# Kernel optimization log

Hardware: AMD Instinct MI355X
Metric: run time of the kernel (lower is better)

The kernel has to match this reference:

```python
import jax, jax.numpy as jnp
import numpy as np

B, S, D_IN, D_OUT, H = 2, 2048, 1024, 1024, 16
DK = D_OUT // H


def setup_inputs() -> dict:
    key = jax.random.key(0)
    ks = jax.random.split(key, 6)
    s_in = 1.0 / np.sqrt(D_IN)
    s_out = 1.0 / np.sqrt(D_OUT)
    return {
        "x": jax.random.normal(ks[0], (B, S, D_IN), dtype=jnp.float32),
        "Wq": jax.random.uniform(ks[1], (D_OUT, D_IN), jnp.float32, -s_in, s_in),
        "Wk": jax.random.uniform(ks[2], (D_OUT, D_IN), jnp.float32, -s_in, s_in),
        "Wv": jax.random.uniform(ks[3], (D_OUT, D_IN), jnp.float32, -s_in, s_in),
        "Wo": jax.random.uniform(ks[4], (D_OUT, D_OUT), jnp.float32, -s_out, s_out),
        "bo": jax.random.uniform(ks[5], (D_OUT,), jnp.float32, -s_out, s_out),
    }


def reference(x, Wq, Wk, Wv, Wo, bo):
    b, s, _ = x.shape
    # torch Linear: y = x @ W.T
    q = (x @ Wq.T).reshape(b, s, H, DK).transpose(0, 2, 1, 3)  # [b,h,s,dk]
    k = (x @ Wk.T).reshape(b, s, H, DK).transpose(0, 2, 1, 3)
    v = (x @ Wv.T).reshape(b, s, H, DK).transpose(0, 2, 1, 3)
    scores = jnp.einsum("bhqd,bhkd->bhqk", q, k)
    causal = jnp.tril(jnp.ones((s, s), dtype=bool))  # True = keep
    scores = jnp.where(causal, scores, -jnp.inf)
    attn = jax.nn.softmax(scores / np.sqrt(DK), axis=-1)
    # dropout p=0.0 (eval) -> identity
    ctx = jnp.einsum("bhqk,bhkd->bhqd", attn, v)
    ctx = ctx.transpose(0, 2, 1, 3).reshape(b, s, D_OUT)
    return ctx @ Wo.T + bo
```

## Files before the change

kernel.cpp:

```cpp
#include <hip/hip_runtime.h>
#include <stdint.h>

#define B_   2
#define S_   2048
#define DIN  1024
#define DOUT 1024
#define H_   16
#define DK_  64
#define MSZ  (B_ * S_)

typedef __bf16 bf16v8 __attribute__((ext_vector_type(8)));
typedef float  f32x4  __attribute__((ext_vector_type(4)));

__device__ __forceinline__ ushort f2b(float f) {
  union { float f; uint32_t u; } a; a.f = f;
  uint32_t u = a.u;
  u += 0x7FFFu + ((u >> 16) & 1u);
  return (ushort)(u >> 16);
}

__device__ __forceinline__ uint32_t pk2(float lo, float hi) {
  union { __bf16 h; ushort u; } a, b;
  a.h = (__bf16)lo; b.h = (__bf16)hi;
  return (uint32_t)a.u | ((uint32_t)b.u << 16);
}

#define GLDS(gp, lp) __builtin_amdgcn_global_load_lds(                         \
    (const __attribute__((address_space(1))) void*)(gp),                       \
    (__attribute__((address_space(3))) void*)(lp), 16, 0, 0)

__global__ void cvt_all(const float* __restrict__ x,  const float* __restrict__ wq,
                        const float* __restrict__ wk, const float* __restrict__ wv,
                        const float* __restrict__ wo,
                        ushort* __restrict__ xb,  ushort* __restrict__ wqb,
                        ushort* __restrict__ wkb, ushort* __restrict__ wvb,
                        ushort* __restrict__ wob) {
  int i = blockIdx.x * blockDim.x + threadIdx.x;
  const int NX = 1 << 20, NW = 1 << 18;
  const float* src; ushort* dst; int off;
  if (i < NX)               { src = x;  dst = xb;  off = i; }
  else if (i < NX + NW)     { src = wq; dst = wqb; off = i - NX; }
  else if (i < NX + 2 * NW) { src = wk; dst = wkb; off = i - NX - NW; }
  else if (i < NX + 3 * NW) { src = wv; dst = wvb; off = i - NX - 2 * NW; }
  else                      { src = wo; dst = wob; off = i - NX - 3 * NW; }
  float4 v = reinterpret_cast<const float4*>(src)[off];
  ushort4 o;
  o.x = f2b(v.x); o.y = f2b(v.y); o.z = f2b(v.z); o.w = f2b(v.w);
  reinterpret_cast<ushort4*>(dst)[off] = o;
}

__global__ __launch_bounds__(256)
void gemm_qkv(const ushort* __restrict__ A,
              const ushort* __restrict__ Bq, const ushort* __restrict__ Bk,
              const ushort* __restrict__ Bv,
              ushort* __restrict__ Oq, ushort* __restrict__ Ok,
              ushort* __restrict__ Vt, int M, int K) {
  __shared__ ushort sA[128 * 64];
  __shared__ ushort sB[128 * 64];

  const int tid  = threadIdx.x;
  const int lane = tid & 63, wid = tid >> 6;
  const int wr = wid >> 1, wc = wid & 1;
  const int g = lane >> 4, c = lane & 15;
  const int m0 = blockIdx.x * 128;

  const int wsel = blockIdx.y >> 3;
  const int n0w  = (blockIdx.y & 7) * 128;
  const ushort* Bm = (wsel == 0) ? Bq : (wsel == 1) ? Bk : Bv;

  const int msk = (c & 7) << 4;

  f32x4 acc[4][4] = {};

  for (int k0 = 0; k0 < K; k0 += 64) {
    __syncthreads();
#pragma unroll
    for (int i = 0; i < 4; ++i) {
      int idx = i * 256 + tid;
      int row = idx >> 3;
      int scol = (((idx & 7) ^ (row & 7)) << 3);
      GLDS(A  + (size_t)(m0 + row) * K + k0 + scol, (char*)sA + idx * 16);
      GLDS(Bm + (size_t)(n0w + row) * K + k0 + scol, (char*)sB + idx * 16);
    }
    __syncthreads();

    bf16v8 aF[4][2], bF[4][2];
#pragma unroll
    for (int m = 0; m < 4; ++m) {
      const char* rp = (const char*)sA + (wr * 64 + m * 16 + c) * 128;
#pragma unroll
      for (int ks = 0; ks < 2; ++ks)
        aF[m][ks] = *reinterpret_cast<const bf16v8*>(rp + ((ks * 64 + g * 16) ^ msk));
    }
#pragma unroll
    for (int n = 0; n < 4; ++n) {
      const char* rp = (const char*)sB + (wc * 64 + n * 16 + c) * 128;
#pragma unroll
      for (int ks = 0; ks < 2; ++ks)
        bF[n][ks] = *reinterpret_cast<const bf16v8*>(rp + ((ks * 64 + g * 16) ^ msk));
    }
#pragma unroll
    for (int m = 0; m < 4; ++m)
#pragma unroll
      for (int n = 0; n < 4; ++n) {
        acc[m][n] = __builtin_amdgcn_mfma_f32_16x16x32_bf16(aF[m][0], bF[n][0], acc[m][n], 0, 0, 0);
        acc[m][n] = __builtin_amdgcn_mfma_f32_16x16x32_bf16(aF[m][1], bF[n][1], acc[m][n], 0, 0, 0);
      }
  }

  __syncthreads();

  if (wsel == 2) {
#pragma unroll
    for (int m = 0; m < 4; ++m)
#pragma unroll
      for (int n = 0; n < 4; ++n) {
        int row0 = m0 + wr * 64 + g * 4 + m * 16;
        int col  = n0w + wc * 64 + c + n * 16;
        int bb = row0 >> 11, ss = row0 & 2047;
        int hh = col >> 6, dd = col & 63;
        ushort4 o4;
        o4.x = f2b(acc[m][n][0]); o4.y = f2b(acc[m][n][1]);
        o4.z = f2b(acc[m][n][2]); o4.w = f2b(acc[m][n][3]);
        *reinterpret_cast<ushort4*>(
            &Vt[((size_t)(bb * 16 + hh) * 64 + dd) * 2048 + ss]) = o4;
      }
  } else {
    const float oscale = (wsel == 0) ? 0.125f * 1.4426950408889634f : 1.0f;
    ushort* Ob = (wsel == 0) ? Oq : Ok;
    char* eb = (char*)sA + wid * 2048;
#pragma unroll
    for (int m = 0; m < 4; ++m) {
#pragma unroll
      for (int n = 0; n < 4; ++n)
#pragma unroll
        for (int i = 0; i < 4; ++i) {
          int prow = g * 4 + i;
          *(ushort*)(eb + prow * 128 + ((n * 32 + c * 2) ^ ((prow & 7) << 4))) =
              f2b(acc[m][n][i] * oscale);
        }
      const int r = lane >> 2, cq = lane & 3;
      const int m2 = (r & 7) << 4;
      bf16v8 t0 = *reinterpret_cast<const bf16v8*>(eb + r * 128 + ((cq * 32) ^ m2));
      bf16v8 t1 = *reinterpret_cast<const bf16v8*>(eb + r * 128 + ((cq * 32 + 16) ^ m2));
      ushort* Gb = Ob + (size_t)(m0 + wr * 64 + m * 16 + r) * DOUT +
                   n0w + wc * 64 + cq * 16;
      *reinterpret_cast<bf16v8*>(Gb) = t0;
      *reinterpret_cast<bf16v8*>(Gb + 8) = t1;
    }
  }
}

__global__ __launch_bounds__(256)
void gemm_proj(const ushort* __restrict__ A, const ushort* __restrict__ Bw,
               float* __restrict__ Cf, const float* __restrict__ bias,
               int M, int K) {
  __shared__ ushort sAB[2][64 * 64];

  const int tid  = threadIdx.x;
  const int lane = tid & 63, wid = tid >> 6;
  const int wr = wid >> 1, wc = wid & 1;
  const int g = lane >> 4, c = lane & 15;
  const int m0 = blockIdx.x * 64, n0 = blockIdx.y * 64;

  const int msk = (c & 7) << 4;

  f32x4 acc[2][2] = {};

  for (int k0 = 0; k0 < K; k0 += 64) {
    __syncthreads();
#pragma unroll
    for (int i = 0; i < 2; ++i) {
      int idx = i * 256 + tid;
      int row = idx >> 3;
      int scol = (((idx & 7) ^ (row & 7)) << 3);
      GLDS(A  + (size_t)(m0 + row) * K + k0 + scol, (char*)&sAB[0][0] + idx * 16);
      GLDS(Bw + (size_t)(n0 + row) * K + k0 + scol, (char*)&sAB[1][0] + idx * 16);
    }
    __syncthreads();

    bf16v8 aF[2][2], bF[2][2];
#pragma unroll
    for (int m = 0; m < 2; ++m) {
      const char* rp = (const char*)&sAB[0][0] + (wr * 32 + m * 16 + c) * 128;
#pragma unroll
      for (int ks = 0; ks < 2; ++ks)
        aF[m][ks] = *reinterpret_cast<const bf16v8*>(rp + ((ks * 64 + g * 16) ^ msk));
    }
#pragma unroll
    for (int n = 0; n < 2; ++n) {
      const char* rp = (const char*)&sAB[1][0] + (wc * 32 + n * 16 + c) * 128;
#pragma unroll
      for (int ks = 0; ks < 2; ++ks)
        bF[n][ks] = *reinterpret_cast<const bf16v8*>(rp + ((ks * 64 + g * 16) ^ msk));
    }
#pragma unroll
    for (int m = 0; m < 2; ++m)
#pragma unroll
      for (int n = 0; n < 2; ++n) {
        acc[m][n] = __builtin_amdgcn_mfma_f32_16x16x32_bf16(aF[m][0], bF[n][0], acc[m][n], 0, 0, 0);
        acc[m][n] = __builtin_amdgcn_mfma_f32_16x16x32_bf16(aF[m][1], bF[n][1], acc[m][n], 0, 0, 0);
      }
  }

  __syncthreads();

  float bv[2];
#pragma unroll
  for (int n = 0; n < 2; ++n) bv[n] = bias[n0 + wc * 32 + n * 16 + c];

  float* ef = (float*)((char*)&sAB[0][0] + wid * 4096);
#pragma unroll
  for (int m = 0; m < 2; ++m)
#pragma unroll
    for (int n = 0; n < 2; ++n)
#pragma unroll
      for (int i = 0; i < 4; ++i) {
        int row = m * 16 + g * 4 + i;
        ef[row * 32 + ((n * 16 + c) ^ ((row & 7) << 2))] = acc[m][n][i] + bv[n];
      }
#pragma unroll
  for (int pass = 0; pass < 4; ++pass) {
    int idx = pass * 64 + lane;
    int row = idx >> 3, q = idx & 7;
    float4 v = *reinterpret_cast<const float4*>(
        &ef[row * 32 + ((q * 4) ^ ((row & 7) << 2))]);
    *reinterpret_cast<float4*>(
        &Cf[(size_t)(m0 + wr * 32 + row) * DOUT + n0 + wc * 32 + q * 4]) = v;
  }
}

__global__ __launch_bounds__(512)
void flash_attn(const ushort* __restrict__ Q, const ushort* __restrict__ K,
                const ushort* __restrict__ Vt, ushort* __restrict__ O) {
  __shared__ ushort sK[2][128][64];
  __shared__ ushort sV[2][64][128];
  __shared__ ushort sP[8][16][64];

  const int tid  = threadIdx.x;
  const int lane = tid & 63, wid = tid >> 6;
  const int wid4 = wid & 3;
  const int g = lane >> 4, c = lane & 15;

  const int orig = blockIdx.x;
  const int xcd  = orig & 7, idc = orig >> 3;
  const int bh   = xcd * 4 + (idc >> 4);
  const int tp   = idc & 15;
  const int b = bh >> 4, h = bh & 15;
  const int q0    = (wid < 4) ? tp * 64 : (31 - tp) * 64;
  const int q0max = (31 - tp) * 64;

  const ushort* Qb = Q  + (size_t)b * S_ * DOUT + h * DK_;
  const ushort* Kb = K  + (size_t)b * S_ * DOUT + h * DK_;
  const ushort* Vb = Vt + (size_t)bh * DK_ * S_;

  const int msk  = (c & 7) << 4;
  const int pswz = (c & 7) << 2;

  const int kr0 = tid >> 3,        kc0 = ((tid & 7) ^ (kr0 & 7)) << 3;
  const int kr1 = (tid + 512) >> 3, kc1 = (((tid + 512) & 7) ^ (kr1 & 7)) << 3;
  const int vd0 = tid >> 4,        vh0 = (tid >> 3) & 1;
  const int vc0 = ((tid & 7) ^ (vd0 & 7)) << 3;
  const int vd1 = (tid + 512) >> 4, vh1 = ((tid + 512) >> 3) & 1;
  const int vc1 = (((tid + 512) & 7) ^ (vd1 & 7)) << 3;

  bf16v8 qf[2];
  {
    const ushort* qrow = Qb + (size_t)(q0 + wid4 * 16 + c) * DOUT;
    qf[0] = *reinterpret_cast<const bf16v8*>(qrow + g * 8);
    qf[1] = *reinterpret_cast<const bf16v8*>(qrow + 32 + g * 8);
  }

  bf16v8 ones;
#pragma unroll
  for (int j = 0; j < 8; ++j) ones[j] = (__bf16)1.0f;

  GLDS(Kb + (size_t)kr0 * DOUT + kc0, (char*)&sK[0][0][0] + tid * 16);
  GLDS(Kb + (size_t)kr1 * DOUT + kc1, (char*)&sK[0][0][0] + (tid + 512) * 16);
  GLDS(Vb + (size_t)vd0 * S_ + vh0 * 64 + vc0, (char*)&sV[0][0][0] + tid * 16);
  GLDS(Vb + (size_t)vd1 * S_ + vh1 * 64 + vc1, (char*)&sV[0][0][0] + (tid + 512) * 16);
  __syncthreads();

  f32x4 accO[4] = {};
  f32x4 accL = {};
  char* sPw = (char*)&sP[wid][0][0];
  const int qg = q0 + wid4 * 16 + c;
  const int qdiag = q0 + wid4 * 16;

  int buf = 0;
  for (int kv0 = 0; kv0 <= q0max; kv0 += 128, buf ^= 1) {
    if (kv0 + 128 <= q0max) {
      const int nb = buf ^ 1, kvn = kv0 + 128;
      GLDS(Kb + (size_t)(kvn + kr0) * DOUT + kc0, (char*)&sK[nb][0][0] + tid * 16);
      GLDS(Kb + (size_t)(kvn + kr1) * DOUT + kc1, (char*)&sK[nb][0][0] + (tid + 512) * 16);
      GLDS(Vb + (size_t)vd0 * S_ + kvn + vh0 * 64 + vc0, (char*)&sV[nb][0][0] + tid * 16);
      GLDS(Vb + (size_t)vd1 * S_ + kvn + vh1 * 64 + vc1, (char*)&sV[nb][0][0] + (tid + 512) * 16);
    }

#pragma unroll
    for (int sub = 0; sub < 2; ++sub) {
      const int kvs = kv0 + sub * 64;
      if (kvs <= q0) {
        const char* cK = (const char*)&sK[buf][0][0] + sub * (64 * 128);
        const char* cV = (const char*)&sV[buf][0][0] + sub * 128;

        f32x4 s[4] = {};
        __builtin_amdgcn_s_setprio(1);
#pragma unroll
        for (int nf = 0; nf < 4; ++nf) {
          const char* rp = cK + (nf * 16 + c) * 128;
#pragma unroll
          for (int ks = 0; ks < 2; ++ks) {
            bf16v8 kf = *reinterpret_cast<const bf16v8*>(rp + ((ks * 64 + g * 16) ^ msk));
            s[nf] = __builtin_amdgcn_mfma_f32_16x16x32_bf16(kf, qf[ks], s[nf], 0, 0, 0);
          }
        }
        __builtin_amdgcn_s_setprio(0);

        if (kvs + 63 > qdiag) {
#pragma unroll
          for (int nf = 0; nf < 4; ++nf)
#pragma unroll
            for (int i = 0; i < 4; ++i)
              if (kvs + nf * 16 + g * 4 + i > qg) s[nf][i] = -1e30f;
        }

#pragma unroll
        for (int nf = 0; nf < 4; ++nf) {
          float p0 = exp2f(s[nf][0]), p1 = exp2f(s[nf][1]);
          float p2 = exp2f(s[nf][2]), p3 = exp2f(s[nf][3]);
          uint2 w2; w2.x = pk2(p0, p1); w2.y = pk2(p2, p3);
          *reinterpret_cast<uint2*>(
              sPw + c * 128 + (((nf * 8 + g * 2) ^ pswz) << 2)) = w2;
        }
        bf16v8 pf[2];
#pragma unroll
        for (int ks = 0; ks < 2; ++ks)
          pf[ks] = *reinterpret_cast<const bf16v8*>(
              sPw + c * 128 + (((ks * 16 + g * 4) ^ pswz) << 2));

        __builtin_amdgcn_s_setprio(1);
#pragma unroll
        for (int ks = 0; ks < 2; ++ks)
          accL = __builtin_amdgcn_mfma_f32_16x16x32_bf16(pf[ks], ones, accL, 0, 0, 0);
#pragma unroll
        for (int nf2 = 0; nf2 < 4; ++nf2) {
          const char* vp = cV + (nf2 * 16 + c) * 256;
#pragma unroll
          for (int ks = 0; ks < 2; ++ks) {
            bf16v8 vf = *reinterpret_cast<const bf16v8*>(vp + ((ks * 64 + g * 16) ^ msk));
            accO[nf2] = __builtin_amdgcn_mfma_f32_16x16x32_bf16(pf[ks], vf, accO[nf2], 0, 0, 0);
          }
        }
        __builtin_amdgcn_s_setprio(0);
      }
    }

    __syncthreads();
  }

#pragma unroll
  for (int nf = 0; nf < 4; ++nf)
#pragma unroll
    for (int i = 0; i < 4; ++i) {
      int prow = g * 4 + i;
      float v = accO[nf][i] / accL[i];
      *(ushort*)(sPw + prow * 128 +
                 ((nf * 32 + c * 2) ^ ((prow & 7) << 4))) = f2b(v);
    }
  {
    const int r = lane >> 2, cq = lane & 3;
    const char* base = sPw + r * 128;
    const int m2 = (r & 7) << 4;
    bf16v8 t0 = *reinterpret_cast<const bf16v8*>(base + ((cq * 32) ^ m2));
    bf16v8 t1 = *reinterpret_cast<const bf16v8*>(base + ((cq * 32 + 16) ^ m2));
    ushort* Gb = O + (size_t)b * S_ * DOUT +
                 (size_t)(q0 + wid4 * 16 + r) * DOUT + h * DK_ + cq * 16;
    *reinterpret_cast<bf16v8*>(Gb) = t0;
    *reinterpret_cast<bf16v8*>(Gb + 8) = t1;
  }
}

extern "C" void kernel_launch(void* const* d_in, const int* in_sizes, int n_in,
                              void* d_out, int out_size, void* d_ws, size_t ws_size,
                              hipStream_t stream) {
  const float* x  = (const float*)d_in[0];
  const float* Wq = (const float*)d_in[1];
  const float* Wk = (const float*)d_in[2];
  const float* Wv = (const float*)d_in[3];
  const float* Wo = (const float*)d_in[4];
  const float* bo = (const float*)d_in[5];
  float* out = (float*)d_out;

  char* ws = (char*)d_ws;
  const size_t MB = (size_t)1 << 20;
  ushort* xb  = (ushort*)(ws);
  ushort* wqb = (ushort*)(ws +  8 * MB);
  ushort* wkb = (ushort*)(ws + 10 * MB);
  ushort* wvb = (ushort*)(ws + 12 * MB);
  ushort* wob = (ushort*)(ws + 14 * MB);
  ushort* qb  = (ushort*)(ws + 16 * MB);
  ushort* kb  = (ushort*)(ws + 24 * MB);
  ushort* vtb = (ushort*)(ws + 32 * MB);
  ushort* cb  = (ushort*)(ws);

  const int ncv = (1 << 20) + 4 * (1 << 18);
  cvt_all<<<ncv / 256, 256, 0, stream>>>(x, Wq, Wk, Wv, Wo,
                                         xb, wqb, wkb, wvb, wob);

  dim3 gqkv(MSZ / 128, 24, 1);
  gemm_qkv<<<gqkv, 256, 0, stream>>>(xb, wqb, wkb, wvb, qb, kb, vtb,
                                     MSZ, DIN);

  flash_attn<<<B_ * H_ * (S_ / 128), 512, 0, stream>>>(qb, kb, vtb, cb);

  dim3 gproj(MSZ / 64, DOUT / 64, 1);
  gemm_proj<<<gproj, 256, 0, stream>>>(cb, wob, out, bo, MSZ, DOUT);
}
```

Before: 107.2 us.

## Rewrite flash attention with 32x32 MFMA and in-register P transpose

The attention kernel moves from 8 waves of 16-row tiles using 16x16x32 MFMAs to 4 waves of 32-row tiles using 32x32x16 MFMAs. The probability matrix P now stays in registers, rearranged with v_permlane32_swap, instead of round-tripping through LDS. The row sum is accumulated in scalar registers instead of through an extra MFMA against a ones vector. This removes LDS traffic and MFMA work for the normalizer, but halves the waves per block, raises register pressure, and relies on the new permlane layout being correct.

```diff
diff --git a/kernel.cpp b/kernel.cpp
--- a/kernel.cpp
+++ b/kernel.cpp
@@ -11,6 +11,7 @@
 
 typedef __bf16 bf16v8 __attribute__((ext_vector_type(8)));
 typedef float  f32x4  __attribute__((ext_vector_type(4)));
+typedef float  f32x16 __attribute__((ext_vector_type(16)));
 
 __device__ __forceinline__ ushort f2b(float f) {
   union { float f; uint32_t u; } a; a.f = f;
@@ -23,6 +24,10 @@
   union { __bf16 h; ushort u; } a, b;
   a.h = (__bf16)lo; b.h = (__bf16)hi;
   return (uint32_t)a.u | ((uint32_t)b.u << 16);
+}
+
+__device__ __forceinline__ void pl32swap(uint32_t& a, uint32_t& b) {
+  asm("v_permlane32_swap_b32 %0, %1" : "+v"(a), "+v"(b));
 }
 
 #define GLDS(gp, lp) __builtin_amdgcn_global_load_lds(                         \
@@ -230,154 +235,152 @@
   }
 }
 
-__global__ __launch_bounds__(512)
+__global__ __launch_bounds__(256)
 void flash_attn(const ushort* __restrict__ Q, const ushort* __restrict__ K,
                 const ushort* __restrict__ Vt, ushort* __restrict__ O) {
   __shared__ ushort sK[2][128][64];
   __shared__ ushort sV[2][64][128];
-  __shared__ ushort sP[8][16][64];
 
   const int tid  = threadIdx.x;
   const int lane = tid & 63, wid = tid >> 6;
-  const int wid4 = wid & 3;
-  const int g = lane >> 4, c = lane & 15;
+  const int r  = lane & 31, hi = lane >> 5;
 
   const int orig = blockIdx.x;
   const int xcd  = orig & 7, idc = orig >> 3;
   const int bh   = xcd * 4 + (idc >> 4);
   const int tp   = idc & 15;
   const int b = bh >> 4, h = bh & 15;
-  const int q0    = (wid < 4) ? tp * 64 : (31 - tp) * 64;
-  const int q0max = (31 - tp) * 64;
+  const int q0w    = ((wid < 2) ? tp : 31 - tp) * 64 + (wid & 1) * 32;
+  const int q0maxB = (31 - tp) * 64 + 63;
+  const int qmax_w = q0w + 31;
 
   const ushort* Qb = Q  + (size_t)b * S_ * DOUT + h * DK_;
   const ushort* Kb = K  + (size_t)b * S_ * DOUT + h * DK_;
   const ushort* Vb = Vt + (size_t)bh * DK_ * S_;
 
-  const int msk  = (c & 7) << 4;
-  const int pswz = (c & 7) << 2;
-
-  const int kr0 = tid >> 3,        kc0 = ((tid & 7) ^ (kr0 & 7)) << 3;
-  const int kr1 = (tid + 512) >> 3, kc1 = (((tid + 512) & 7) ^ (kr1 & 7)) << 3;
-  const int vd0 = tid >> 4,        vh0 = (tid >> 3) & 1;
-  const int vc0 = ((tid & 7) ^ (vd0 & 7)) << 3;
-  const int vd1 = (tid + 512) >> 4, vh1 = ((tid + 512) >> 3) & 1;
-  const int vc1 = (((tid + 512) & 7) ^ (vd1 & 7)) << 3;
-
-  bf16v8 qf[2];
+  bf16v8 qf[4];
   {
-    const ushort* qrow = Qb + (size_t)(q0 + wid4 * 16 + c) * DOUT;
-    qf[0] = *reinterpret_cast<const bf16v8*>(qrow + g * 8);
-    qf[1] = *reinterpret_cast<const bf16v8*>(qrow + 32 + g * 8);
-  }
-
-  bf16v8 ones;
-#pragma unroll
-  for (int j = 0; j < 8; ++j) ones[j] = (__bf16)1.0f;
-
-  GLDS(Kb + (size_t)kr0 * DOUT + kc0, (char*)&sK[0][0][0] + tid * 16);
-  GLDS(Kb + (size_t)kr1 * DOUT + kc1, (char*)&sK[0][0][0] + (tid + 512) * 16);
-  GLDS(Vb + (size_t)vd0 * S_ + vh0 * 64 + vc0, (char*)&sV[0][0][0] + tid * 16);
-  GLDS(Vb + (size_t)vd1 * S_ + vh1 * 64 + vc1, (char*)&sV[0][0][0] + (tid + 512) * 16);
+    const ushort* qrow = Qb + (size_t)(q0w + r) * DOUT + hi * 8;
+#pragma unroll
+    for (int w = 0; w < 4; ++w)
+      qf[w] = *reinterpret_cast<const bf16v8*>(qrow + w * 16);
+  }
+
+#pragma unroll
+  for (int it = 0; it < 4; ++it) {
+    int idx = it * 256 + tid;
+    int krow = idx >> 3, kch = idx & 7;
+    GLDS(Kb + (size_t)krow * DOUT + ((kch ^ (krow & 7)) << 3),
+         (char*)&sK[0][0][0] + idx * 16);
+    int vd = idx >> 4, vhalf = (idx >> 3) & 1, vch = idx & 7;
+    GLDS(Vb + (size_t)vd * S_ + vhalf * 64 + ((vch ^ (vd & 7)) << 3),
+         (char*)&sV[0][0][0] + idx * 16);
+  }
   __syncthreads();
 
-  f32x4 accO[4] = {};
-  f32x4 accL = {};
-  char* sPw = (char*)&sP[wid][0][0];
-  const int qg = q0 + wid4 * 16 + c;
-  const int qdiag = q0 + wid4 * 16;
+  f32x16 accO0 = {}, accO1 = {};
+  float lsumP = 0.0f;
 
   int buf = 0;
-  for (int kv0 = 0; kv0 <= q0max; kv0 += 128, buf ^= 1) {
-    if (kv0 + 128 <= q0max) {
+  for (int kv0 = 0; kv0 <= q0maxB; kv0 += 128, buf ^= 1) {
+    if (kv0 + 128 <= q0maxB) {
       const int nb = buf ^ 1, kvn = kv0 + 128;
-      GLDS(Kb + (size_t)(kvn + kr0) * DOUT + kc0, (char*)&sK[nb][0][0] + tid * 16);
-      GLDS(Kb + (size_t)(kvn + kr1) * DOUT + kc1, (char*)&sK[nb][0][0] + (tid + 512) * 16);
-      GLDS(Vb + (size_t)vd0 * S_ + kvn + vh0 * 64 + vc0, (char*)&sV[nb][0][0] + tid * 16);
-      GLDS(Vb + (size_t)vd1 * S_ + kvn + vh1 * 64 + vc1, (char*)&sV[nb][0][0] + (tid + 512) * 16);
-    }
-
-#pragma unroll
-    for (int sub = 0; sub < 2; ++sub) {
-      const int kvs = kv0 + sub * 64;
-      if (kvs <= q0) {
-        const char* cK = (const char*)&sK[buf][0][0] + sub * (64 * 128);
-        const char* cV = (const char*)&sV[buf][0][0] + sub * 128;
-
-        f32x4 s[4] = {};
+#pragma unroll
+      for (int it = 0; it < 4; ++it) {
+        int idx = it * 256 + tid;
+        int krow = idx >> 3, kch = idx & 7;
+        GLDS(Kb + (size_t)(kvn + krow) * DOUT + ((kch ^ (krow & 7)) << 3),
+             (char*)&sK[nb][0][0] + idx * 16);
+        int vd = idx >> 4, vhalf = (idx >> 3) & 1, vch = idx & 7;
+        GLDS(Vb + (size_t)vd * S_ + kvn + vhalf * 64 + ((vch ^ (vd & 7)) << 3),
+             (char*)&sV[nb][0][0] + idx * 16);
+      }
+    }
+
+    const char* cK = (const char*)&sK[buf][0][0];
+    const char* cV = (const char*)&sV[buf][0][0];
+
+#pragma unroll
+    for (int c4 = 0; c4 < 4; ++c4) {
+      const int kvs = kv0 + c4 * 32;
+      if (kvs <= qmax_w) {
+        f32x16 s = {};
         __builtin_amdgcn_s_setprio(1);
 #pragma unroll
-        for (int nf = 0; nf < 4; ++nf) {
-          const char* rp = cK + (nf * 16 + c) * 128;
-#pragma unroll
-          for (int ks = 0; ks < 2; ++ks) {
-            bf16v8 kf = *reinterpret_cast<const bf16v8*>(rp + ((ks * 64 + g * 16) ^ msk));
-            s[nf] = __builtin_amdgcn_mfma_f32_16x16x32_bf16(kf, qf[ks], s[nf], 0, 0, 0);
+        for (int w = 0; w < 4; ++w) {
+          bf16v8 kf = *reinterpret_cast<const bf16v8*>(
+              cK + (c4 * 32 + r) * 128 + (((w * 2 + hi) ^ (r & 7)) << 4));
+          s = __builtin_amdgcn_mfma_f32_32x32x16_bf16(kf, qf[w], s, 0, 0, 0);
+        }
+        __builtin_amdgcn_s_setprio(0);
+
+        if (kvs + 31 > q0w) {
+#pragma unroll
+          for (int i = 0; i < 16; ++i) {
+            int kv = kvs + (i & 3) + 8 * (i >> 2) + 4 * hi;
+            if (kv > q0w + r) s[i] = -1e30f;
           }
         }
-        __builtin_amdgcn_s_setprio(0);
-
-        if (kvs + 63 > qdiag) {
-#pragma unroll
-          for (int nf = 0; nf < 4; ++nf)
-#pragma unroll
-            for (int i = 0; i < 4; ++i)
-              if (kvs + nf * 16 + g * 4 + i > qg) s[nf][i] = -1e30f;
+
+        uint32_t P32[8];
+#pragma unroll
+        for (int m = 0; m < 4; ++m) {
+          float e0 = exp2f(s[4 * m + 0]), e1 = exp2f(s[4 * m + 1]);
+          float e2 = exp2f(s[4 * m + 2]), e3 = exp2f(s[4 * m + 3]);
+          lsumP += (e0 + e1) + (e2 + e3);
+          P32[2 * m]     = pk2(e0, e1);
+          P32[2 * m + 1] = pk2(e2, e3);
         }
 
 #pragma unroll
-        for (int nf = 0; nf < 4; ++nf) {
-          float p0 = exp2f(s[nf][0]), p1 = exp2f(s[nf][1]);
-          float p2 = exp2f(s[nf][2]), p3 = exp2f(s[nf][3]);
-          uint2 w2; w2.x = pk2(p0, p1); w2.y = pk2(p2, p3);
-          *reinterpret_cast<uint2*>(
-              sPw + c * 128 + (((nf * 8 + g * 2) ^ pswz) << 2)) = w2;
+        for (int w = 0; w < 2; ++w) {
+          uint32_t a0 = P32[4 * w],     a1 = P32[4 * w + 1];
+          uint32_t b0 = P32[4 * w + 2], b1 = P32[4 * w + 3];
+          pl32swap(a0, b0);
+          pl32swap(a1, b1);
+          union { uint32_t u[4]; bf16v8 v; } pu;
+          pu.u[0] = a0; pu.u[1] = a1; pu.u[2] = b0; pu.u[3] = b1;
+          bf16v8 pa = pu.v;
+
+          const int vslot = ((c4 & 1) * 4 + w * 2 + hi) ^ (r & 7);
+          const int vbase = (c4 >> 1) * 128 + (vslot << 4);
+          bf16v8 vf0 = *reinterpret_cast<const bf16v8*>(cV + (r) * 256 + vbase);
+          bf16v8 vf1 = *reinterpret_cast<const bf16v8*>(cV + (32 + r) * 256 + vbase);
+          __builtin_amdgcn_s_setprio(1);
+          accO0 = __builtin_amdgcn_mfma_f32_32x32x16_bf16(pa, vf0, accO0, 0, 0, 0);
+          accO1 = __builtin_amdgcn_mfma_f32_32x32x16_bf16(pa, vf1, accO1, 0, 0, 0);
+          __builtin_amdgcn_s_setprio(0);
         }
-        bf16v8 pf[2];
-#pragma unroll
-        for (int ks = 0; ks < 2; ++ks)
-          pf[ks] = *reinterpret_cast<const bf16v8*>(
-              sPw + c * 128 + (((ks * 16 + g * 4) ^ pswz) << 2));
-
-        __builtin_amdgcn_s_setprio(1);
-#pragma unroll
-        for (int ks = 0; ks < 2; ++ks)
-          accL = __builtin_amdgcn_mfma_f32_16x16x32_bf16(pf[ks], ones, accL, 0, 0, 0);
-#pragma unroll
-        for (int nf2 = 0; nf2 < 4; ++nf2) {
-          const char* vp = cV + (nf2 * 16 + c) * 256;
-#pragma unroll
-          for (int ks = 0; ks < 2; ++ks) {
-            bf16v8 vf = *reinterpret_cast<const bf16v8*>(vp + ((ks * 64 + g * 16) ^ msk));
-            accO[nf2] = __builtin_amdgcn_mfma_f32_16x16x32_bf16(pf[ks], vf, accO[nf2], 0, 0, 0);
-          }
-        }
-        __builtin_amdgcn_s_setprio(0);
       }
     }
 
     __syncthreads();
   }
 
-#pragma unroll
-  for (int nf = 0; nf < 4; ++nf)
-#pragma unroll
-    for (int i = 0; i < 4; ++i) {
-      int prow = g * 4 + i;
-      float v = accO[nf][i] / accL[i];
-      *(ushort*)(sPw + prow * 128 +
-                 ((nf * 32 + c * 2) ^ ((prow & 7) << 4))) = f2b(v);
-    }
-  {
-    const int r = lane >> 2, cq = lane & 3;
-    const char* base = sPw + r * 128;
-    const int m2 = (r & 7) << 4;
-    bf16v8 t0 = *reinterpret_cast<const bf16v8*>(base + ((cq * 32) ^ m2));
-    bf16v8 t1 = *reinterpret_cast<const bf16v8*>(base + ((cq * 32 + 16) ^ m2));
-    ushort* Gb = O + (size_t)b * S_ * DOUT +
-                 (size_t)(q0 + wid4 * 16 + r) * DOUT + h * DK_ + cq * 16;
-    *reinterpret_cast<bf16v8*>(Gb) = t0;
-    *reinterpret_cast<bf16v8*>(Gb + 8) = t1;
+  float lsum = lsumP + __shfl_xor(lsumP, 32);
+  float rinv = 1.0f / lsum;
+
+  __syncthreads();
+
+  char* epi = (char*)&sK[0][0][0] + wid * 4096;
+#pragma unroll
+  for (int i = 0; i < 16; ++i) {
+    const int rc = (i & 3) + 8 * (i >> 2);
+    const int row = rc + 4 * hi;
+    const float rl = __shfl(rinv, rc + 4 * hi);
+    const int xm = (row & 7) << 4;
+    *(ushort*)(epi + row * 128 + ((2 * r) ^ xm))      = f2b(accO0[i] * rl);
+    *(ushort*)(epi + row * 128 + ((64 + 2 * r) ^ xm)) = f2b(accO1[i] * rl);
+  }
+  ushort* Gb = O + (size_t)b * S_ * DOUT + h * DK_;
+#pragma unroll
+  for (int p = 0; p < 4; ++p) {
+    int idx = p * 64 + lane;
+    int row = idx >> 3, slot = idx & 7;
+    bf16v8 t = *reinterpret_cast<const bf16v8*>(
+        epi + row * 128 + ((slot ^ (row & 7)) << 4));
+    *reinterpret_cast<bf16v8*>(
+        Gb + (size_t)(q0w + row) * DOUT + slot * 8) = t;
   }
 }
 
@@ -412,7 +415,7 @@
   gemm_qkv<<<gqkv, 256, 0, stream>>>(xb, wqb, wkb, wvb, qb, kb, vtb,
                                      MSZ, DIN);
 
-  flash_attn<<<B_ * H_ * (S_ / 128), 512, 0, stream>>>(qb, kb, vtb, cb);
+  flash_attn<<<B_ * H_ * (S_ / 128), 256, 0, stream>>>(qb, kb, vtb, cb);
 
   dim3 gproj(MSZ / 64, DOUT / 64, 1);
   gemm_proj<<<gproj, 256, 0, stream>>>(cb, wob, out, bo, MSZ, DOUT);
```

New measurement: 133.9 us. +24.9%, slower.

## Process both causal query tiles per wave in flash attention with 256 threads

Applied to the files above, without the earlier changes.

Each of 4 waves now handles two 16-row query tiles (the low and the mirrored high tile) instead of 8 waves each handling one. K and V fragments are loaded from LDS once into registers and reused by both query chains, halving LDS fragment reads per MFMA. The cost is more registers per wave (two sets of accumulators plus preloaded K/V fragments) and half the waves per block, which reduces latency hiding and doubles the global-to-LDS staging work per thread.

```diff
diff --git a/kernel.cpp b/kernel.cpp
--- a/kernel.cpp
+++ b/kernel.cpp
@@ -230,16 +230,15 @@
   }
 }
 
-__global__ __launch_bounds__(512)
+__global__ __launch_bounds__(256)
 void flash_attn(const ushort* __restrict__ Q, const ushort* __restrict__ K,
                 const ushort* __restrict__ Vt, ushort* __restrict__ O) {
   __shared__ ushort sK[2][128][64];
   __shared__ ushort sV[2][64][128];
-  __shared__ ushort sP[8][16][64];
+  __shared__ ushort sP[4][2][16][64];
 
   const int tid  = threadIdx.x;
   const int lane = tid & 63, wid = tid >> 6;
-  const int wid4 = wid & 3;
   const int g = lane >> 4, c = lane & 15;
 
   const int orig = blockIdx.x;
@@ -247,8 +246,7 @@
   const int bh   = xcd * 4 + (idc >> 4);
   const int tp   = idc & 15;
   const int b = bh >> 4, h = bh & 15;
-  const int q0    = (wid < 4) ? tp * 64 : (31 - tp) * 64;
-  const int q0max = (31 - tp) * 64;
+  const int q0a = tp * 64, q0b = (31 - tp) * 64;
 
   const ushort* Qb = Q  + (size_t)b * S_ * DOUT + h * DK_;
   const ushort* Kb = K  + (size_t)b * S_ * DOUT + h * DK_;
@@ -257,128 +255,144 @@
   const int msk  = (c & 7) << 4;
   const int pswz = (c & 7) << 2;
 
-  const int kr0 = tid >> 3,        kc0 = ((tid & 7) ^ (kr0 & 7)) << 3;
-  const int kr1 = (tid + 512) >> 3, kc1 = (((tid + 512) & 7) ^ (kr1 & 7)) << 3;
-  const int vd0 = tid >> 4,        vh0 = (tid >> 3) & 1;
-  const int vc0 = ((tid & 7) ^ (vd0 & 7)) << 3;
-  const int vd1 = (tid + 512) >> 4, vh1 = ((tid + 512) >> 3) & 1;
-  const int vc1 = (((tid + 512) & 7) ^ (vd1 & 7)) << 3;
-
-  bf16v8 qf[2];
+  bf16v8 qfa[2], qfb[2];
   {
-    const ushort* qrow = Qb + (size_t)(q0 + wid4 * 16 + c) * DOUT;
-    qf[0] = *reinterpret_cast<const bf16v8*>(qrow + g * 8);
-    qf[1] = *reinterpret_cast<const bf16v8*>(qrow + 32 + g * 8);
+    const ushort* qa  = Qb + (size_t)(q0a + wid * 16 + c) * DOUT;
+    const ushort* qb2 = Qb + (size_t)(q0b + wid * 16 + c) * DOUT;
+    qfa[0] = *reinterpret_cast<const bf16v8*>(qa + g * 8);
+    qfa[1] = *reinterpret_cast<const bf16v8*>(qa + 32 + g * 8);
+    qfb[0] = *reinterpret_cast<const bf16v8*>(qb2 + g * 8);
+    qfb[1] = *reinterpret_cast<const bf16v8*>(qb2 + 32 + g * 8);
   }
 
   bf16v8 ones;
 #pragma unroll
   for (int j = 0; j < 8; ++j) ones[j] = (__bf16)1.0f;
 
-  GLDS(Kb + (size_t)kr0 * DOUT + kc0, (char*)&sK[0][0][0] + tid * 16);
-  GLDS(Kb + (size_t)kr1 * DOUT + kc1, (char*)&sK[0][0][0] + (tid + 512) * 16);
-  GLDS(Vb + (size_t)vd0 * S_ + vh0 * 64 + vc0, (char*)&sV[0][0][0] + tid * 16);
-  GLDS(Vb + (size_t)vd1 * S_ + vh1 * 64 + vc1, (char*)&sV[0][0][0] + (tid + 512) * 16);
+#define STAGE(BUFI, KVN)                                                       \
+  {                                                                            \
+    _Pragma("unroll")                                                          \
+    for (int it = 0; it < 4; ++it) {                                           \
+      int idx = it * 256 + tid;                                                \
+      int krow = idx >> 3, kch = idx & 7;                                      \
+      GLDS(Kb + (size_t)((KVN) + krow) * DOUT + ((kch ^ (krow & 7)) << 3),     \
+           (char*)&sK[BUFI][0][0] + idx * 16);                                 \
+      int vd = idx >> 4, vhalf = (idx >> 3) & 1, vch = idx & 7;                \
+      GLDS(Vb + (size_t)vd * S_ + (KVN) + vhalf * 64 + ((vch ^ (vd & 7)) << 3),\
+           (char*)&sV[BUFI][0][0] + idx * 16);                                 \
+    }                                                                          \
+  }
+
+  STAGE(0, 0);
   __syncthreads();
 
-  f32x4 accO[4] = {};
-  f32x4 accL = {};
-  char* sPw = (char*)&sP[wid][0][0];
-  const int qg = q0 + wid4 * 16 + c;
-  const int qdiag = q0 + wid4 * 16;
+  f32x4 accOa[4] = {}, accOb[4] = {};
+  f32x4 accLa = {}, accLb = {};
+  char* sPa = (char*)&sP[wid][0][0][0];
+  char* sPb = (char*)&sP[wid][1][0][0];
+  const int qga = q0a + wid * 16 + c, qdia = q0a + wid * 16;
+  const int qgb = q0b + wid * 16 + c, qdib = q0b + wid * 16;
 
   int buf = 0;
-  for (int kv0 = 0; kv0 <= q0max; kv0 += 128, buf ^= 1) {
-    if (kv0 + 128 <= q0max) {
-      const int nb = buf ^ 1, kvn = kv0 + 128;
-      GLDS(Kb + (size_t)(kvn + kr0) * DOUT + kc0, (char*)&sK[nb][0][0] + tid * 16);
-      GLDS(Kb + (size_t)(kvn + kr1) * DOUT + kc1, (char*)&sK[nb][0][0] + (tid + 512) * 16);
-      GLDS(Vb + (size_t)vd0 * S_ + kvn + vh0 * 64 + vc0, (char*)&sV[nb][0][0] + tid * 16);
-      GLDS(Vb + (size_t)vd1 * S_ + kvn + vh1 * 64 + vc1, (char*)&sV[nb][0][0] + (tid + 512) * 16);
-    }
+  for (int kv0 = 0; kv0 <= q0b; kv0 += 128, buf ^= 1) {
+    if (kv0 + 128 <= q0b) STAGE(buf ^ 1, kv0 + 128);
 
 #pragma unroll
     for (int sub = 0; sub < 2; ++sub) {
       const int kvs = kv0 + sub * 64;
-      if (kvs <= q0) {
-        const char* cK = (const char*)&sK[buf][0][0] + sub * (64 * 128);
+      if (kvs <= q0b) {
+        const char* cK = (const char*)&sK[buf][0][0] + sub * 8192;
         const char* cV = (const char*)&sV[buf][0][0] + sub * 128;
 
-        f32x4 s[4] = {};
-        __builtin_amdgcn_s_setprio(1);
+        bf16v8 kf[4][2], vf[4][2];
 #pragma unroll
         for (int nf = 0; nf < 4; ++nf) {
           const char* rp = cK + (nf * 16 + c) * 128;
+          const char* vp = cV + (nf * 16 + c) * 256;
 #pragma unroll
           for (int ks = 0; ks < 2; ++ks) {
-            bf16v8 kf = *reinterpret_cast<const bf16v8*>(rp + ((ks * 64 + g * 16) ^ msk));
-            s[nf] = __builtin_amdgcn_mfma_f32_16x16x32_bf16(kf, qf[ks], s[nf], 0, 0, 0);
+            kf[nf][ks] = *reinterpret_cast<const bf16v8*>(rp + ((ks * 64 + g * 16) ^ msk));
+            vf[nf][ks] = *reinterpret_cast<const bf16v8*>(vp + ((ks * 64 + g * 16) ^ msk));
           }
         }
-        __builtin_amdgcn_s_setprio(0);
-
-        if (kvs + 63 > qdiag) {
-#pragma unroll
-          for (int nf = 0; nf < 4; ++nf)
-#pragma unroll
-            for (int i = 0; i < 4; ++i)
-              if (kvs + nf * 16 + g * 4 + i > qg) s[nf][i] = -1e30f;
-        }
-
-#pragma unroll
-        for (int nf = 0; nf < 4; ++nf) {
-          float p0 = exp2f(s[nf][0]), p1 = exp2f(s[nf][1]);
-          float p2 = exp2f(s[nf][2]), p3 = exp2f(s[nf][3]);
-          uint2 w2; w2.x = pk2(p0, p1); w2.y = pk2(p2, p3);
-          *reinterpret_cast<uint2*>(
-              sPw + c * 128 + (((nf * 8 + g * 2) ^ pswz) << 2)) = w2;
-        }
-        bf16v8 pf[2];
-#pragma unroll
-        for (int ks = 0; ks < 2; ++ks)
-          pf[ks] = *reinterpret_cast<const bf16v8*>(
-              sPw + c * 128 + (((ks * 16 + g * 4) ^ pswz) << 2));
-
-        __builtin_amdgcn_s_setprio(1);
-#pragma unroll
-        for (int ks = 0; ks < 2; ++ks)
-          accL = __builtin_amdgcn_mfma_f32_16x16x32_bf16(pf[ks], ones, accL, 0, 0, 0);
-#pragma unroll
-        for (int nf2 = 0; nf2 < 4; ++nf2) {
-          const char* vp = cV + (nf2 * 16 + c) * 256;
-#pragma unroll
-          for (int ks = 0; ks < 2; ++ks) {
-            bf16v8 vf = *reinterpret_cast<const bf16v8*>(vp + ((ks * 64 + g * 16) ^ msk));
-            accO[nf2] = __builtin_amdgcn_mfma_f32_16x16x32_bf16(pf[ks], vf, accO[nf2], 0, 0, 0);
+
+        auto chain = [&](const bf16v8* qf, f32x4* accO, f32x4& accL,
+                         int qg, int qdiag, char* sPt) {
+          f32x4 s[4] = {};
+          __builtin_amdgcn_s_setprio(1);
+#pragma unroll
+          for (int nf = 0; nf < 4; ++nf) {
+            s[nf] = __builtin_amdgcn_mfma_f32_16x16x32_bf16(kf[nf][0], qf[0], s[nf], 0, 0, 0);
+            s[nf] = __builtin_amdgcn_mfma_f32_16x16x32_bf16(kf[nf][1], qf[1], s[nf], 0, 0, 0);
           }
-        }
-        __builtin_amdgcn_s_setprio(0);
+          __builtin_amdgcn_s_setprio(0);
+
+          if (kvs + 63 > qdiag) {
+#pragma unroll
+            for (int nf = 0; nf < 4; ++nf)
+#pragma unroll
+              for (int i = 0; i < 4; ++i)
+                if (kvs + nf * 16 + g * 4 + i > qg) s[nf][i] = -1e30f;
+          }
+
+          char* pbase = sPt + c * 128;
+#pragma unroll
+          for (int nf = 0; nf < 4; ++nf) {
+            float p0 = exp2f(s[nf][0]), p1 = exp2f(s[nf][1]);
+            float p2 = exp2f(s[nf][2]), p3 = exp2f(s[nf][3]);
+            uint2 w2; w2.x = pk2(p0, p1); w2.y = pk2(p2, p3);
+            *reinterpret_cast<uint2*>(
+                pbase + (((nf * 8 + g * 2) ^ pswz) << 2)) = w2;
+          }
+          bf16v8 pf[2];
+#pragma unroll
+          for (int ks = 0; ks < 2; ++ks)
+            pf[ks] = *reinterpret_cast<const bf16v8*>(
+                pbase + (((ks * 16 + g * 4) ^ pswz) << 2));
+
+          __builtin_amdgcn_s_setprio(1);
+#pragma unroll
+          for (int ks = 0; ks < 2; ++ks)
+            accL = __builtin_amdgcn_mfma_f32_16x16x32_bf16(pf[ks], ones, accL, 0, 0, 0);
+#pragma unroll
+          for (int nf2 = 0; nf2 < 4; ++nf2) {
+            accO[nf2] = __builtin_amdgcn_mfma_f32_16x16x32_bf16(pf[0], vf[nf2][0], accO[nf2], 0, 0, 0);
+            accO[nf2] = __builtin_amdgcn_mfma_f32_16x16x32_bf16(pf[1], vf[nf2][1], accO[nf2], 0, 0, 0);
+          }
+          __builtin_amdgcn_s_setprio(0);
+        };
+
+        if (kvs <= q0a) chain(qfa, accOa, accLa, qga, qdia, sPa);
+        chain(qfb, accOb, accLb, qgb, qdib, sPb);
       }
     }
 
     __syncthreads();
   }
-
-#pragma unroll
-  for (int nf = 0; nf < 4; ++nf)
-#pragma unroll
-    for (int i = 0; i < 4; ++i) {
-      int prow = g * 4 + i;
-      float v = accO[nf][i] / accL[i];
-      *(ushort*)(sPw + prow * 128 +
-                 ((nf * 32 + c * 2) ^ ((prow & 7) << 4))) = f2b(v);
-    }
-  {
+#undef STAGE
+
+  auto epi = [&](f32x4* accO, f32x4& accL, int q0x, char* sPt) {
+#pragma unroll
+    for (int nf = 0; nf < 4; ++nf)
+#pragma unroll
+      for (int i = 0; i < 4; ++i) {
+        int prow = g * 4 + i;
+        float v = accO[nf][i] / accL[i];
+        *(ushort*)(sPt + prow * 128 +
+                   ((nf * 32 + c * 2) ^ ((prow & 7) << 4))) = f2b(v);
+      }
     const int r = lane >> 2, cq = lane & 3;
-    const char* base = sPw + r * 128;
+    const char* base = sPt + r * 128;
     const int m2 = (r & 7) << 4;
     bf16v8 t0 = *reinterpret_cast<const bf16v8*>(base + ((cq * 32) ^ m2));
     bf16v8 t1 = *reinterpret_cast<const bf16v8*>(base + ((cq * 32 + 16) ^ m2));
     ushort* Gb = O + (size_t)b * S_ * DOUT +
-                 (size_t)(q0 + wid4 * 16 + r) * DOUT + h * DK_ + cq * 16;
+                 (size_t)(q0x + wid * 16 + r) * DOUT + h * DK_ + cq * 16;
     *reinterpret_cast<bf16v8*>(Gb) = t0;
     *reinterpret_cast<bf16v8*>(Gb + 8) = t1;
-  }
+  };
+  epi(accOa, accLa, q0a, sPa);
+  epi(accOb, accLb, q0b, sPb);
 }
 
 extern "C" void kernel_launch(void* const* d_in, const int* in_sizes, int n_in,
@@ -412,7 +426,7 @@
   gemm_qkv<<<gqkv, 256, 0, stream>>>(xb, wqb, wkb, wvb, qb, kb, vtb,
                                      MSZ, DIN);
 
-  flash_attn<<<B_ * H_ * (S_ / 128), 512, 0, stream>>>(qb, kb, vtb, cb);
+  flash_attn<<<B_ * H_ * (S_ / 128), 256, 0, stream>>>(qb, kb, vtb, cb);
 
   dim3 gproj(MSZ / 64, DOUT / 64, 1);
   gemm_proj<<<gproj, 256, 0, stream>>>(cb, wob, out, bo, MSZ, DOUT);
```

Measured after the change: 136.6 us. 27.4% more time.
